# Performance work log

Hardware: AMD Instinct MI355X
Metric: run time of the kernel (lower is better)

The kernel has to match this reference:

```python
import jax, jax.numpy as jnp
import numpy as np

B, N, D, H_IMG, W_IMG = 1, 6, 128, 28, 60
HB, WB = 50, 50
HEADS, DH = 4, 32
INNER = HEADS * DH  # 128 == D
Q = HB * WB
NK = N * H_IMG * W_IMG


def _ln(x, w, b, eps=1e-5):
    m = jnp.mean(x, axis=-1, keepdims=True)
    v = jnp.var(x, axis=-1, keepdims=True)
    return (x - m) * jax.lax.rsqrt(v + eps) * w + b


def setup_inputs() -> dict:
    key = jax.random.key(0)
    ks = jax.random.split(key, 20)
    s = 0.02
    inp = {
        "q": jax.random.normal(ks[0], (B, D, HB, WB), jnp.float32),
        "k": jax.random.normal(ks[1], (B, N, D, H_IMG, W_IMG), jnp.float32),
        "v": jax.random.normal(ks[2], (B, N, D, H_IMG, W_IMG), jnp.float32),
        "W_logits": jax.random.uniform(ks[3], (B, Q, NK), jnp.float32),
        "vis_flat": jax.random.randint(ks[4], (B, Q, NK), 0, 2).astype(jnp.int32),
        "skip": jax.random.normal(ks[5], (B, D, HB, WB), jnp.float32),
        # LayerNorm params
        "qn_w": jnp.ones((D,), jnp.float32), "qn_b": jnp.zeros((D,), jnp.float32),
        "kn_w": jnp.ones((D,), jnp.float32), "kn_b": jnp.zeros((D,), jnp.float32),
        "vn_w": jnp.ones((D,), jnp.float32), "vn_b": jnp.zeros((D,), jnp.float32),
        "pre_w": jnp.ones((D,), jnp.float32), "pre_b": jnp.zeros((D,), jnp.float32),
        "post_w": jnp.ones((D,), jnp.float32), "post_b": jnp.zeros((D,), jnp.float32),
        # Linear params, stored [in, out]
        "wq": jax.random.normal(ks[6], (D, INNER), jnp.float32) * s,
        "bq": jnp.zeros((INNER,), jnp.float32),
        "wk": jax.random.normal(ks[7], (D, INNER), jnp.float32) * s,
        "bk": jnp.zeros((INNER,), jnp.float32),
        "wv": jax.random.normal(ks[8], (D, INNER), jnp.float32) * s,
        "bv": jnp.zeros((INNER,), jnp.float32),
        "wp": jax.random.normal(ks[9], (INNER, D), jnp.float32) * s,
        "bp": jnp.zeros((D,), jnp.float32),
        "w1": jax.random.normal(ks[10], (D, 2 * D), jnp.float32) * s,
        "b1": jnp.zeros((2 * D,), jnp.float32),
        "w2": jax.random.normal(ks[11], (2 * D, D), jnp.float32) * s,
        "b2": jnp.zeros((D,), jnp.float32),
    }
    return inp


def reference(q, k, v, W_logits, vis_flat, skip,
              qn_w, qn_b, kn_w, kn_b, vn_w, vn_b, pre_w, pre_b, post_w, post_b,
              wq, bq, wk, bk, wv, bv, wp, bp, w1, b1, w2, b2):
    b, d, Hb, Wb = q.shape
    _, n, _, hi, wi = k.shape
    Qn = Hb * Wb
    # b d H W -> b (H W) d ; b n d h w -> b (n h w) d
    qf = q.reshape(b, d, Qn).transpose(0, 2, 1)
    kf = k.transpose(0, 1, 3, 4, 2).reshape(b, n * hi * wi, d)
    vf = v.transpose(0, 1, 3, 4, 2).reshape(b, n * hi * wi, d)
    qf = _ln(qf, qn_w, qn_b)
    kf = _ln(kf, kn_w, kn_b)
    vf = _ln(vf, vn_w, vn_b)
    qh = (qf @ wq + bq).reshape(b, Qn, HEADS, DH).transpose(0, 2, 1, 3)
    kh = (kf @ wk + bk).reshape(b, -1, HEADS, DH).transpose(0, 2, 1, 3)
    vh = (vf @ wv + bv).reshape(b, -1, HEADS, DH).transpose(0, 2, 1, 3)
    scale = DH ** (-0.5)
    logits = jnp.einsum('bhqd,bhkd->bhqk', qh, kh) * scale  # [b,h,Q,NK]
    neg_inf = jnp.finfo(logits.dtype).min
    logits = jnp.where(vis_flat[:, None] == 0, neg_inf, logits)
    logits = logits * W_logits[:, None]  # multiplicative EAF weighting
    attn = jax.nn.softmax(logits, axis=-1)
    out = jnp.einsum('bhqk,bhkd->bhqd', attn, vh)
    out = out.transpose(0, 2, 1, 3).reshape(b, Qn, INNER)
    out = out @ wp + bp
    z = out + skip.reshape(b, d, Qn).transpose(0, 2, 1)
    z = _ln(z, pre_w, pre_b)
    z = z + (jax.nn.gelu(z @ w1 + b1, approximate=False) @ w2 + b2)
    z = _ln(z, post_w, post_b)
    return z.transpose(0, 2, 1).reshape(b, d, Hb, Wb)
```

## Files before the change

### kernel.cpp

```cpp
#include <hip/hip_runtime.h>
#include <hip/hip_bf16.h>
#include <math.h>

typedef short short8 __attribute__((ext_vector_type(8)));
typedef float floatx4 __attribute__((ext_vector_type(4)));
typedef int   intx4  __attribute__((ext_vector_type(4)));

#define D 128
#define Q 2500
#define QPAD 2560
#define NK 10080
#define NKPAD 10112
#define SPLITS 19
#define CPS 17
#define OPS 163904
#define LPS 10304
#define VBW 320
#define VROW 40
#define QSCALE 0.25501268426834347f
#define NEGBIG -3.0e38f

__device__ __forceinline__ unsigned short f2bf(float f) {
    unsigned u = __float_as_uint(f);
    unsigned r = (u + 0x7fffu + ((u >> 16) & 1u)) >> 16;
    return (unsigned short)r;
}
__device__ __forceinline__ unsigned pack2bf(float lo, float hi) {
    unsigned u0 = __float_as_uint(lo) + 0x8000u;
    unsigned u1 = __float_as_uint(hi) + 0x8000u;
    return (u0 >> 16) | (u1 & 0xffff0000u);
}
__device__ __forceinline__ float bflo(unsigned u) { return __uint_as_float(u << 16); }
__device__ __forceinline__ float bfhi(unsigned u) { return __uint_as_float(u & 0xffff0000u); }

__global__ __launch_bounds__(256) void prep_kernel(
    const float* __restrict__ qi, const float* __restrict__ ki, const float* __restrict__ vi,
    const float* __restrict__ qw, const float* __restrict__ qb_,
    const float* __restrict__ kw, const float* __restrict__ kb,
    const float* __restrict__ vw, const float* __restrict__ vb,
    unsigned short* __restrict__ xq, unsigned short* __restrict__ xk,
    unsigned short* __restrict__ xv,
    const float* __restrict__ wq, const float* __restrict__ wk,
    const float* __restrict__ wv, const float* __restrict__ wp,
    const float* __restrict__ w1, const float* __restrict__ w2,
    unsigned short* __restrict__ wqT, unsigned short* __restrict__ wkT,
    unsigned short* __restrict__ wvT, unsigned short* __restrict__ wpT,
    unsigned short* __restrict__ w1T, unsigned short* __restrict__ w2T,
    const int* __restrict__ vis, unsigned* __restrict__ vbits) {
    int bid = blockIdx.x, t = threadIdx.x;
    if (bid >= 1227) {
        int row = bid - 1227;
        const int* src = vis + (size_t)row * NK;
        #pragma unroll 2
        for (int w = t; w < 315; w += 256) {
            unsigned bits = 0;
            const intx4* p = (const intx4*)(src + w * 32);
            #pragma unroll
            for (int g = 0; g < 8; g++) {
                intx4 v = p[g];
                #pragma unroll
                for (int j = 0; j < 4; j++) bits |= (v[j] ? 1u : 0u) << (g * 4 + j);
            }
            vbits[(size_t)row * VBW + w] = bits;
        }
        return;
    }
    if (bid >= 715) {
        int idx = (bid - 715) * 256 + t;
        if (idx < 49152) {
            int m = idx >> 14;
            int local = idx & 16383;
            int n = local >> 7, kk = local & 127;
            const float* w = (m == 0) ? wq : ((m == 1) ? wk : wv);
            unsigned short* o = (m == 0) ? wqT : ((m == 1) ? wkT : wvT);
            o[local] = f2bf(w[kk * 128 + n]);
        } else if (idx < 65536) {
            int local = idx - 49152;
            int n = local >> 7, kk = local & 127;
            wpT[local] = f2bf(wp[kk * 128 + n]);
        } else if (idx < 98304) {
            int local = idx - 65536;
            int n = local >> 7, kk = local & 127;
            w1T[local] = f2bf(w1[kk * 256 + n]);
        } else {
            int local = idx - 98304;
            int n = local >> 8, kk = local & 255;
            w2T[local] = f2bf(w2[kk * 128 + n]);
        }
        return;
    }
    __shared__ float lds2[32 * 132];
    const float* src; unsigned short* dst; const float *g, *b;
    int S, valid;
    if (bid < 79) {
        int p0 = bid * 32;
        src = qi + p0; S = Q; dst = xq + p0 * D; g = qw; b = qb_;
        valid = Q - p0; if (valid > 32) valid = 32;
    } else if (bid < 397) {
        int tt = bid - 79;
        int n = tt / 53, tile = tt - n * 53, r = tile * 32;
        src = ki + (size_t)(n * 128) * 1680 + r; S = 1680;
        dst = xk + (n * 1680 + r) * D; g = kw; b = kb;
        valid = 1680 - r; if (valid > 32) valid = 32;
    } else {
        int tt = bid - 397;
        int n = tt / 53, tile = tt - n * 53, r = tile * 32;
        src = vi + (size_t)(n * 128) * 1680 + r; S = 1680;
        dst = xv + (n * 1680 + r) * D; g = vw; b = vb;
        valid = 1680 - r; if (valid > 32) valid = 32;
    }
    #pragma unroll
    for (int pass = 0; pass < 4; pass++) {
        int s = pass * 256 + t;
        int d = s >> 3, ps = s & 7;
        floatx4 val = {0.f, 0.f, 0.f, 0.f};
        if (ps * 4 < valid) val = *(const floatx4*)(src + (size_t)d * S + ps * 4);
        #pragma unroll
        for (int j = 0; j < 4; j++) lds2[(ps * 4 + j) * 132 + d] = val[j];
    }
    __syncthreads();
    int lane = t & 63, wvx = t >> 6;
    int pos = wvx * 8 + (lane >> 3), l7 = lane & 7;
    floatx4 x4[4];
    #pragma unroll
    for (int k = 0; k < 4; k++) x4[k] = *(const floatx4*)(&lds2[pos * 132 + l7 * 16 + k * 4]);
    float s = 0.f, ss = 0.f;
    #pragma unroll
    for (int k = 0; k < 4; k++)
        #pragma unroll
        for (int j = 0; j < 4; j++) { s += x4[k][j]; ss += x4[k][j] * x4[k][j]; }
    #pragma unroll
    for (int m = 1; m <= 4; m <<= 1) { s += __shfl_xor(s, m, 64); ss += __shfl_xor(ss, m, 64); }
    float mean = s * (1.0f / 128.0f);
    float var = ss * (1.0f / 128.0f) - mean * mean;
    float rstd = rsqrtf(var + 1e-5f);
    short8 o1, o2;
    #pragma unroll
    for (int k = 0; k < 4; k++) {
        floatx4 g4 = *(const floatx4*)(g + l7 * 16 + k * 4);
        floatx4 b4 = *(const floatx4*)(b + l7 * 16 + k * 4);
        #pragma unroll
        for (int j = 0; j < 4; j++) {
            float o = (x4[k][j] - mean) * rstd * g4[j] + b4[j];
            if (k < 2) o1[k * 4 + j] = (short)f2bf(o);
            else o2[(k - 2) * 4 + j] = (short)f2bf(o);
        }
    }
    if (pos < valid) {
        *(short8*)(dst + pos * D + l7 * 16) = o1;
        *(short8*)(dst + pos * D + l7 * 16 + 8) = o2;
    }
}

__global__ __launch_bounds__(256) void proj_kernel(
    const unsigned short* __restrict__ xq, const unsigned short* __restrict__ xk,
    const unsigned short* __restrict__ xv,
    const unsigned short* __restrict__ wqT, const unsigned short* __restrict__ wkT,
    const unsigned short* __restrict__ wvT,
    const float* __restrict__ bq, const float* __restrict__ bk, const float* __restrict__ bv,
    unsigned short* __restrict__ qh, unsigned short* __restrict__ kh,
    unsigned short* __restrict__ vhT) {
    __shared__ short vlds[128 * 72];
    int bid = blockIdx.x;
    const unsigned short *src, *wT; const float* bias; int mb, mode; float scale;
    if (bid < 40)       { mode = 0; src = xq; wT = wqT; bias = bq; mb = bid * 64; scale = QSCALE; }
    else if (bid < 198) { mode = 1; src = xk; wT = wkT; bias = bk; mb = (bid - 40) * 64; scale = 1.0f; }
    else                { mode = 2; src = xv; wT = wvT; bias = bv; mb = (bid - 198) * 64; scale = 1.0f; }
    int t = threadIdx.x, wave = t >> 6, lane = t & 63;
    int l15 = lane & 15, quad = lane >> 4;
    int m0 = mb + wave * 16;
    floatx4 acc[8];
    #pragma unroll
    for (int i = 0; i < 8; i++) acc[i] = (floatx4){0.f, 0.f, 0.f, 0.f};
    #pragma unroll
    for (int kf = 0; kf < 4; kf++) {
        short8 A = *(const short8*)(src + (m0 + l15) * D + kf * 32 + quad * 8);
        #pragma unroll
        for (int nt = 0; nt < 8; nt++) {
            short8 Bv = *(const short8*)(wT + (nt * 16 + l15) * D + kf * 32 + quad * 8);
            acc[nt] = __builtin_amdgcn_mfma_f32_16x16x32_bf16(A, Bv, acc[nt], 0, 0, 0);
        }
    }
    if (mode != 2) {
        unsigned short* dst = (mode == 0) ? qh : kh;
        #pragma unroll
        for (int nt = 0; nt < 8; nt++) {
            float bb = bias[nt * 16 + l15];
            #pragma unroll
            for (int r = 0; r < 4; r++)
                dst[(m0 + quad * 4 + r) * D + nt * 16 + l15] = f2bf((acc[nt][r] + bb) * scale);
        }
    } else {
        #pragma unroll
        for (int nt = 0; nt < 8; nt++) {
            float bb = bias[nt * 16 + l15];
            #pragma unroll
            for (int r = 0; r < 4; r++)
                vlds[(nt * 16 + l15) * 72 + (wave * 16 + quad * 4 + r)] =
                    (short)f2bf(acc[nt][r] + bb);
        }
        __syncthreads();
        int pr = t & 31, dd = t >> 5;
        int sub = pr >> 4, i = pr & 15;
        #pragma unroll
        for (int pass = 0; pass < 16; pass++) {
            int d = pass * 8 + dd;
            unsigned lo = (unsigned short)vlds[d * 72 + sub * 32 + i];
            unsigned hi = (unsigned short)vlds[d * 72 + sub * 32 + 16 + i];
            *(unsigned*)(vhT + (size_t)d * NKPAD + mb + sub * 32 + 2 * i) = lo | (hi << 16);
        }
    }
}

template<int USEBITS>
__global__ __launch_bounds__(256, 3) void attn_kernel_t(
    const unsigned short* __restrict__ qh, const unsigned short* __restrict__ kh,
    const unsigned short* __restrict__ vhT,
    const float* __restrict__ Wl, const int* __restrict__ vis,
    const unsigned* __restrict__ vbits,
    unsigned* __restrict__ OpartU, float* __restrict__ lpart) {
    __shared__ short Kl[2][32 * 136];
    __shared__ short Vl[2][128 * VROW];
    __shared__ unsigned Pl[4][16 * 18];
    int bid = blockIdx.x;
    int split = bid % SPLITS, qt = bid / SPLITS;
    int t = threadIdx.x, wave = t >> 6, lane = t & 63;
    int l15 = lane & 15, quad = lane >> 4;
    int qb = qt * 64 + wave * 16;
    int k00 = split * (CPS * 32);
    int cmax = (NK - k00) >> 5; if (cmax > CPS) cmax = CPS;

    short8 qB[4];
    #pragma unroll
    for (int h = 0; h < 4; h++)
        qB[h] = *(const short8*)(qh + (size_t)(qb + l15) * D + h * 32 + quad * 8);

    int kr = t >> 3, ks = (t & 7) * 2;
    int vd = t >> 1, vs = (t & 1) * 2;
    const uint4* ksrc = (const uint4*)(kh + (size_t)(k00 + kr) * D + ks * 8);
    const uint4* vsrc = (const uint4*)(vhT + (size_t)vd * NKPAD + k00 + vs * 8);
    short* kdst = &Kl[0][kr * 136 + ks * 8];
    short* vdst = &Vl[0][vd * VROW + vs * 8];

    int wrow = qb + l15; if (wrow >= Q) wrow = Q - 1;
    const float* wp = Wl + (size_t)wrow * NK + k00 + quad * 4;
    const int*   vp = vis + (size_t)wrow * NK + k00 + quad * 4;
    const unsigned* vbp = vbits + (size_t)wrow * VBW + split * CPS;

    const floatx4 zf = {0.f, 0.f, 0.f, 0.f};
    floatx4 O[4][2];
    float lacc[4];
    #pragma unroll
    for (int h = 0; h < 4; h++) { O[h][0] = zf; O[h][1] = zf; lacc[h] = 0.f; }

    uint4 ka = ksrc[0], kb2 = ksrc[1];
    uint4 va = vsrc[0], vb2 = vsrc[1];
    floatx4 wc0 = *(const floatx4*)wp;
    floatx4 wc1 = *(const floatx4*)(wp + 16);
    intx4 vc0, vc1;
    unsigned vbc = 0;
    if constexpr (USEBITS) {
        vbc = vbp[0];
    } else {
        vc0 = *(const intx4*)vp;
        vc1 = *(const intx4*)(vp + 16);
    }
    *(uint4*)kdst = ka;       *(uint4*)(kdst + 8) = kb2;
    *(uint4*)vdst = va;       *(uint4*)(vdst + 8) = vb2;

    unsigned* pw = Pl[wave];
    #pragma unroll 1
    for (int c = 0; c < cmax; c++) {
        __syncthreads();
        int buf = c & 1;
        uint4 nka, nkb, nva, nvb;
        floatx4 wn0, wn1; intx4 vn0, vn1;
        unsigned vbn = 0;
        if (c + 1 < cmax) {
            const uint4* ks2 = ksrc + (size_t)(c + 1) * 512;
            const uint4* vs2 = vsrc + (size_t)(c + 1) * 4;
            nka = ks2[0]; nkb = ks2[1];
            nva = vs2[0]; nvb = vs2[1];
            wn0 = *(const floatx4*)(wp + (c + 1) * 32);
            wn1 = *(const floatx4*)(wp + (c + 1) * 32 + 16);
            if constexpr (USEBITS) {
                vbn = vbp[c + 1];
            } else {
                vn0 = *(const intx4*)(vp + (c + 1) * 32);
                vn1 = *(const intx4*)(vp + (c + 1) * 32 + 16);
            }
        }
        float a2[8], b2[8];
        if constexpr (USEBITS) {
            unsigned bq = vbc >> (quad * 4);
            #pragma unroll
            for (int r = 0; r < 4; r++) {
                bool m0 = (bq >> r) & 1u;
                bool m1 = (bq >> (16 + r)) & 1u;
                a2[r]     = m0 ? wc0[r] : 0.f;
                b2[r]     = m0 ? 0.f : wc0[r] * NEGBIG;
                a2[4 + r] = m1 ? wc1[r] : 0.f;
                b2[4 + r] = m1 ? 0.f : wc1[r] * NEGBIG;
            }
        } else {
            #pragma unroll
            for (int r = 0; r < 4; r++) {
                a2[r]     = vc0[r] ? wc0[r] : 0.f;
                b2[r]     = vc0[r] ? 0.f : wc0[r] * NEGBIG;
                a2[4 + r] = vc1[r] ? wc1[r] : 0.f;
                b2[4 + r] = vc1[r] ? 0.f : wc1[r] * NEGBIG;
            }
        }
        const short* Kb = Kl[buf];
        const short* Vb = Vl[buf];
        #pragma unroll
        for (int h = 0; h < 4; h++) {
            short8 kA0 = *(const short8*)(Kb + l15 * 136 + h * 32 + quad * 8);
            short8 kA1 = *(const short8*)(Kb + (16 + l15) * 136 + h * 32 + quad * 8);
            floatx4 S0 = __builtin_amdgcn_mfma_f32_16x16x32_bf16(kA0, qB[h], zf, 0, 0, 0);
            floatx4 S1 = __builtin_amdgcn_mfma_f32_16x16x32_bf16(kA1, qB[h], zf, 0, 0, 0);
            float p0[4], p1[4];
            #pragma unroll
            for (int r = 0; r < 4; r++) {
                p0[r] = exp2f(S0[r] * a2[r] + b2[r]);
                p1[r] = exp2f(S1[r] * a2[4 + r] + b2[4 + r]);
                lacc[h] += p0[r] + p1[r];
            }
            pw[(quad * 2) * 18 + l15]     = pack2bf(p0[0], p0[1]);
            pw[(quad * 2 + 1) * 18 + l15] = pack2bf(p0[2], p0[3]);
            pw[(8 + quad * 2) * 18 + l15]     = pack2bf(p1[0], p1[1]);
            pw[(8 + quad * 2 + 1) * 18 + l15] = pack2bf(p1[2], p1[3]);
            union { unsigned u[4]; short8 s8; } pb;
            #pragma unroll
            for (int jj = 0; jj < 4; jj++)
                pb.u[jj] = pw[(quad * 4 + jj) * 18 + l15];
            short8 vA0 = *(const short8*)(Vb + (h * 32 + l15) * VROW + quad * 8);
            short8 vA1 = *(const short8*)(Vb + (h * 32 + 16 + l15) * VROW + quad * 8);
            O[h][0] = __builtin_amdgcn_mfma_f32_16x16x32_bf16(vA0, pb.s8, O[h][0], 0, 0, 0);
            O[h][1] = __builtin_amdgcn_mfma_f32_16x16x32_bf16(vA1, pb.s8, O[h][1], 0, 0, 0);
        }
        if (c + 1 < cmax) {
            short* kd = buf ? kdst : (kdst + 32 * 136);
            short* vd2 = buf ? vdst : (vdst + 128 * VROW);
            *(uint4*)kd = nka;       *(uint4*)(kd + 8) = nkb;
            *(uint4*)vd2 = nva;      *(uint4*)(vd2 + 8) = nvb;
            wc0 = wn0; wc1 = wn1;
            if constexpr (USEBITS) { vbc = vbn; }
            else { vc0 = vn0; vc1 = vn1; }
        }
    }

    int row = qb + l15;
    #pragma unroll
    for (int h = 0; h < 4; h++) {
        float lv = lacc[h];
        lv += __shfl_xor(lv, 16, 64);
        lv += __shfl_xor(lv, 32, 64);
        if (quad == 0) lpart[(size_t)split * LPS + row * 4 + h] = lv;
        #pragma unroll
        for (int tl = 0; tl < 2; tl++) {
            uint2 o2;
            o2.x = pack2bf(O[h][tl][0], O[h][tl][1]);
            o2.y = pack2bf(O[h][tl][2], O[h][tl][3]);
            *(uint2*)(OpartU + (size_t)split * OPS + ((size_t)row * 4 + h) * 16 + tl * 8 + quad * 2) = o2;
        }
    }
}

__global__ __launch_bounds__(128) void combine_kernel(
    const unsigned* __restrict__ Opart, const float* __restrict__ lpart,
    unsigned* __restrict__ A1u) {
    int tid = blockIdx.x * 128 + threadIdx.x;
    int sl = tid & 3, he = (tid >> 2) & 3, grow = tid >> 4;
    float lsum = 0.f;
    #pragma unroll 5
    for (int sp = 0; sp < SPLITS; sp++) lsum += lpart[(size_t)sp * LPS + grow * 4 + he];
    float inv = 1.0f / fmaxf(lsum, 1e-30f);
    size_t base = ((size_t)grow * 4 + he) * 16 + sl * 4;
    float a0 = 0.f, a1 = 0.f, a2 = 0.f, a3 = 0.f, a4 = 0.f, a5 = 0.f, a6 = 0.f, a7 = 0.f;
    #pragma unroll 5
    for (int sp = 0; sp < SPLITS; sp++) {
        uint4 u = *(const uint4*)(Opart + (size_t)sp * OPS + base);
        a0 += bflo(u.x); a1 += bfhi(u.x);
        a2 += bflo(u.y); a3 += bfhi(u.y);
        a4 += bflo(u.z); a5 += bfhi(u.z);
        a6 += bflo(u.w); a7 += bfhi(u.w);
    }
    uint4 o;
    o.x = pack2bf(a0 * inv, a1 * inv);
    o.y = pack2bf(a2 * inv, a3 * inv);
    o.z = pack2bf(a4 * inv, a5 * inv);
    o.w = pack2bf(a6 * inv, a7 * inv);
    *(uint4*)(A1u + (size_t)grow * 64 + he * 16 + sl * 4) = o;
}

__global__ __launch_bounds__(256) void mlp_kernel(
    const unsigned short* __restrict__ A1,
    const unsigned short* __restrict__ wpT,
    const float* __restrict__ bp, const float* __restrict__ skip,
    const float* __restrict__ pre_w, const float* __restrict__ pre_b,
    const unsigned short* __restrict__ w1T, const float* __restrict__ b1,
    const unsigned short* __restrict__ w2T, const float* __restrict__ b2,
    const float* __restrict__ post_w, const float* __restrict__ post_b,
    float* __restrict__ out) {
    __shared__ __align__(16) char smem[51200];
    short* Z1 = (short*)smem;
    short* H1 = (short*)(smem + 17408);
    float* Zout = (float*)smem;

    int qb = blockIdx.x * 64;
    int t = threadIdx.x, wave = t >> 6, lane = t & 63;
    int l15 = lane & 15, quad = lane >> 4;
    int m0 = wave * 16;

    floatx4 z[8];
    #pragma unroll
    for (int i = 0; i < 8; i++) z[i] = (floatx4){0.f, 0.f, 0.f, 0.f};
    #pragma unroll
    for (int kf = 0; kf < 4; kf++) {
        short8 A = *(const short8*)(A1 + (size_t)(qb + m0 + l15) * 128 + kf * 32 + quad * 8);
        #pragma unroll
        for (int nt = 0; nt < 8; nt++) {
            short8 Bv = *(const short8*)(wpT + (nt * 16 + l15) * D + kf * 32 + quad * 8);
            z[nt] = __builtin_amdgcn_mfma_f32_16x16x32_bf16(A, Bv, z[nt], 0, 0, 0);
        }
    }
    float Zv[8][4];
    #pragma unroll
    for (int nt = 0; nt < 8; nt++) {
        int n = nt * 16 + l15;
        float bb = bp[n];
        #pragma unroll
        for (int r = 0; r < 4; r++) {
            int q = qb + m0 + quad * 4 + r;
            int qc = q < Q ? q : (Q - 1);
            Zv[nt][r] = z[nt][r] + bb + skip[n * Q + qc];
        }
    }
    float Zn[8][4];
    {
        #pragma unroll
        for (int r = 0; r < 4; r++) {
            float s1 = 0.f, s2 = 0.f;
            #pragma unroll
            for (int nt = 0; nt < 8; nt++) { s1 += Zv[nt][r]; s2 += Zv[nt][r] * Zv[nt][r]; }
            #pragma unroll
            for (int m = 1; m <= 8; m <<= 1) { s1 += __shfl_xor(s1, m, 64); s2 += __shfl_xor(s2, m, 64); }
            float mean = s1 * (1.0f / 128.0f);
            float var = s2 * (1.0f / 128.0f) - mean * mean;
            float rstd = rsqrtf(var + 1e-5f);
            #pragma unroll
            for (int nt = 0; nt < 8; nt++) Zn[nt][r] = (Zv[nt][r] - mean) * rstd;
        }
        #pragma unroll
        for (int nt = 0; nt < 8; nt++) {
            int n = nt * 16 + l15;
            float g = pre_w[n], be = pre_b[n];
            #pragma unroll
            for (int r = 0; r < 4; r++) {
                Zn[nt][r] = Zn[nt][r] * g + be;
                Z1[(m0 + quad * 4 + r) * 136 + n] = (short)f2bf(Zn[nt][r]);
            }
        }
    }
    {
        floatx4 h2[16];
        #pragma unroll
        for (int i = 0; i < 16; i++) h2[i] = (floatx4){0.f, 0.f, 0.f, 0.f};
        #pragma unroll
        for (int kf = 0; kf < 4; kf++) {
            short8 A = *(const short8*)(Z1 + (m0 + l15) * 136 + kf * 32 + quad * 8);
            #pragma unroll
            for (int nt = 0; nt < 16; nt++) {
                short8 Bv = *(const short8*)(w1T + (nt * 16 + l15) * D + kf * 32 + quad * 8);
                h2[nt] = __builtin_amdgcn_mfma_f32_16x16x32_bf16(A, Bv, h2[nt], 0, 0, 0);
            }
        }
        #pragma unroll
        for (int nt = 0; nt < 16; nt++) {
            int n = nt * 16 + l15;
            float bb = b1[n];
            #pragma unroll
            for (int r = 0; r < 4; r++) {
                float x = h2[nt][r] + bb;
                float gl = 0.5f * x * (1.0f + erff(x * 0.70710678118654752f));
                H1[(m0 + quad * 4 + r) * 264 + n] = (short)f2bf(gl);
            }
        }
    }
    floatx4 o3[8];
    #pragma unroll
    for (int i = 0; i < 8; i++) o3[i] = (floatx4){0.f, 0.f, 0.f, 0.f};
    #pragma unroll
    for (int kf = 0; kf < 8; kf++) {
        short8 A = *(const short8*)(H1 + (m0 + l15) * 264 + kf * 32 + quad * 8);
        #pragma unroll
        for (int nt = 0; nt < 8; nt++) {
            short8 Bv = *(const short8*)(w2T + (nt * 16 + l15) * 256 + kf * 32 + quad * 8);
            o3[nt] = __builtin_amdgcn_mfma_f32_16x16x32_bf16(A, Bv, o3[nt], 0, 0, 0);
        }
    }
    float Z2[8][4];
    #pragma unroll
    for (int nt = 0; nt < 8; nt++) {
        int n = nt * 16 + l15;
        float bb = b2[n];
        #pragma unroll
        for (int r = 0; r < 4; r++) Z2[nt][r] = Zn[nt][r] + o3[nt][r] + bb;
    }
    float Zo[8][4];
    {
        #pragma unroll
        for (int r = 0; r < 4; r++) {
            float s1 = 0.f, s2 = 0.f;
            #pragma unroll
            for (int nt = 0; nt < 8; nt++) { s1 += Z2[nt][r]; s2 += Z2[nt][r] * Z2[nt][r]; }
            #pragma unroll
            for (int m = 1; m <= 8; m <<= 1) { s1 += __shfl_xor(s1, m, 64); s2 += __shfl_xor(s2, m, 64); }
            float mean = s1 * (1.0f / 128.0f);
            float var = s2 * (1.0f / 128.0f) - mean * mean;
            float rstd = rsqrtf(var + 1e-5f);
            #pragma unroll
            for (int nt = 0; nt < 8; nt++) Zo[nt][r] = (Z2[nt][r] - mean) * rstd;
        }
        #pragma unroll
        for (int nt = 0; nt < 8; nt++) {
            int n = nt * 16 + l15;
            float g = post_w[n], be = post_b[n];
            #pragma unroll
            for (int r = 0; r < 4; r++) Zo[nt][r] = Zo[nt][r] * g + be;
        }
    }
    __syncthreads();
    #pragma unroll
    for (int nt = 0; nt < 8; nt++)
        #pragma unroll
        for (int r = 0; r < 4; r++)
            Zout[(nt * 16 + l15) * 65 + m0 + quad * 4 + r] = Zo[nt][r];
    __syncthreads();
    {
        int pl = t & 63;
        int q = qb + pl;
        if (q < Q) {
            #pragma unroll
            for (int it = 0; it < 32; it++) {
                int n = it * 4 + (t >> 6);
                out[n * Q + q] = Zout[n * 65 + pl];
            }
        }
    }
}

extern "C" void kernel_launch(void* const* d_in, const int* in_sizes, int n_in,
                              void* d_out, int out_size, void* d_ws, size_t ws_size,
                              hipStream_t stream) {
    (void)in_sizes; (void)n_in; (void)out_size;
    const float* q      = (const float*)d_in[0];
    const float* k      = (const float*)d_in[1];
    const float* v      = (const float*)d_in[2];
    const float* Wl     = (const float*)d_in[3];
    const int*   vis    = (const int*)  d_in[4];
    const float* skip   = (const float*)d_in[5];
    const float* qn_w   = (const float*)d_in[6];
    const float* qn_b   = (const float*)d_in[7];
    const float* kn_w   = (const float*)d_in[8];
    const float* kn_b   = (const float*)d_in[9];
    const float* vn_w   = (const float*)d_in[10];
    const float* vn_b   = (const float*)d_in[11];
    const float* pre_w  = (const float*)d_in[12];
    const float* pre_b  = (const float*)d_in[13];
    const float* post_w = (const float*)d_in[14];
    const float* post_b = (const float*)d_in[15];
    const float* wq     = (const float*)d_in[16];
    const float* bq     = (const float*)d_in[17];
    const float* wk     = (const float*)d_in[18];
    const float* bk     = (const float*)d_in[19];
    const float* wv     = (const float*)d_in[20];
    const float* bv     = (const float*)d_in[21];
    const float* wp     = (const float*)d_in[22];
    const float* bp     = (const float*)d_in[23];
    const float* w1     = (const float*)d_in[24];
    const float* b1     = (const float*)d_in[25];
    const float* w2     = (const float*)d_in[26];
    const float* b2     = (const float*)d_in[27];
    float* out = (float*)d_out;

    char* ws = (char*)d_ws;
    unsigned short* xq  = (unsigned short*)(ws + 0);
    unsigned short* xk  = (unsigned short*)(ws + 655360);
    unsigned short* xv  = (unsigned short*)(ws + 3244032);
    unsigned short* qh  = (unsigned short*)(ws + 5832704);
    unsigned short* kh  = (unsigned short*)(ws + 6488064);
    unsigned short* vhT = (unsigned short*)(ws + 9076736);
    unsigned short* wqT = (unsigned short*)(ws + 11665408);
    unsigned short* wkT = (unsigned short*)(ws + 11698176);
    unsigned short* wvT = (unsigned short*)(ws + 11730944);
    unsigned short* wpT = (unsigned short*)(ws + 11763712);
    unsigned short* w1T = (unsigned short*)(ws + 11796480);
    unsigned short* w2T = (unsigned short*)(ws + 11862016);
    unsigned* OpartU    = (unsigned*)(ws + 11927552);
    float* lpart        = (float*)(ws + 34874112);
    unsigned* vbits     = (unsigned*)(ws + 36316672);
    unsigned* A1u       = (unsigned*)(ws + 0);

    const bool usebits = (ws_size == 0) || (ws_size >= 39520000ull);

    prep_kernel<<<dim3(usebits ? 3727 : 1227), dim3(256), 0, stream>>>(
        q, k, v, qn_w, qn_b, kn_w, kn_b, vn_w, vn_b, xq, xk, xv,
        wq, wk, wv, wp, w1, w2, wqT, wkT, wvT, wpT, w1T, w2T, vis, vbits);
    proj_kernel<<<dim3(356), dim3(256), 0, stream>>>(xq, xk, xv, wqT, wkT, wvT, bq, bk, bv,
                                                     qh, kh, vhT);
    if (usebits)
        attn_kernel_t<1><<<dim3(40 * SPLITS), dim3(256), 0, stream>>>(
            qh, kh, vhT, Wl, vis, vbits, OpartU, lpart);
    else
        attn_kernel_t<0><<<dim3(40 * SPLITS), dim3(256), 0, stream>>>(
            qh, kh, vhT, Wl, vis, vbits, OpartU, lpart);
    combine_kernel<<<dim3(320), dim3(128), 0, stream>>>(OpartU, lpart, A1u);
    mlp_kernel<<<dim3(40), dim3(256), 0, stream>>>((const unsigned short*)A1u, wpT, bp, skip,
                                                   pre_w, pre_b, w1T, b1, w2T, b2,
                                                   post_w, post_b, out);
}
```

Baseline: 364.5 us.

## Shuffle P tile in registers and fuse split-combine into MLP kernel

In the attention loop, the per-wave LDS round trip that turned the P tile into an MFMA operand is replaced by hardware bf16 pack instructions and cross-lane shuffles. The separate combine kernel that reduces split partials is folded into the MLP kernel, which reduces into LDS before the projection GEMM. This drops one kernel launch and a global round trip for A1. The trade-off is that the combine now runs on only 40 blocks, which lowers parallelism for that reduction, and the MLP kernel needs more LDS.

```diff
diff --git a/kernel.cpp b/kernel.cpp
--- a/kernel.cpp
+++ b/kernel.cpp
@@ -29,6 +29,11 @@
     unsigned u0 = __float_as_uint(lo) + 0x8000u;
     unsigned u1 = __float_as_uint(hi) + 0x8000u;
     return (u0 >> 16) | (u1 & 0xffff0000u);
+}
+__device__ __forceinline__ unsigned cvtpk(float lo, float hi) {
+    unsigned r;
+    asm("v_cvt_pk_bf16_f32 %0, %1, %2" : "=v"(r) : "v"(lo), "v"(hi));
+    return r;
 }
 __device__ __forceinline__ float bflo(unsigned u) { return __uint_as_float(u << 16); }
 __device__ __forceinline__ float bfhi(unsigned u) { return __uint_as_float(u & 0xffff0000u); }
@@ -221,7 +226,6 @@
     unsigned* __restrict__ OpartU, float* __restrict__ lpart) {
     __shared__ short Kl[2][32 * 136];
     __shared__ short Vl[2][128 * VROW];
-    __shared__ unsigned Pl[4][16 * 18];
     int bid = blockIdx.x;
     int split = bid % SPLITS, qt = bid / SPLITS;
     int t = threadIdx.x, wave = t >> 6, lane = t & 63;
@@ -246,6 +250,10 @@
     const float* wp = Wl + (size_t)wrow * NK + k00 + quad * 4;
     const int*   vp = vis + (size_t)wrow * NK + k00 + quad * 4;
     const unsigned* vbp = vbits + (size_t)wrow * VBW + split * CPS;
+
+    int idxA = l15 + ((quad & 1) << 5);
+    int idxB = idxA + 16;
+    bool hiK = (quad >= 2);
 
     const floatx4 zf = {0.f, 0.f, 0.f, 0.f};
     floatx4 O[4][2];
@@ -268,7 +276,6 @@
     *(uint4*)kdst = ka;       *(uint4*)(kdst + 8) = kb2;
     *(uint4*)vdst = va;       *(uint4*)(vdst + 8) = vb2;
 
-    unsigned* pw = Pl[wave];
     #pragma unroll 1
     for (int c = 0; c < cmax; c++) {
         __syncthreads();
@@ -326,14 +333,19 @@
                 p1[r] = exp2f(S1[r] * a2[4 + r] + b2[4 + r]);
                 lacc[h] += p0[r] + p1[r];
             }
-            pw[(quad * 2) * 18 + l15]     = pack2bf(p0[0], p0[1]);
-            pw[(quad * 2 + 1) * 18 + l15] = pack2bf(p0[2], p0[3]);
-            pw[(8 + quad * 2) * 18 + l15]     = pack2bf(p1[0], p1[1]);
-            pw[(8 + quad * 2 + 1) * 18 + l15] = pack2bf(p1[2], p1[3]);
+            unsigned u0 = cvtpk(p0[0], p0[1]);
+            unsigned u1 = cvtpk(p0[2], p0[3]);
+            unsigned u2 = cvtpk(p1[0], p1[1]);
+            unsigned u3 = cvtpk(p1[2], p1[3]);
+            unsigned s0A = __shfl(u0, idxA, 64), s2A = __shfl(u2, idxA, 64);
+            unsigned s1A = __shfl(u1, idxA, 64), s3A = __shfl(u3, idxA, 64);
+            unsigned s0B = __shfl(u0, idxB, 64), s2B = __shfl(u2, idxB, 64);
+            unsigned s1B = __shfl(u1, idxB, 64), s3B = __shfl(u3, idxB, 64);
             union { unsigned u[4]; short8 s8; } pb;
-            #pragma unroll
-            for (int jj = 0; jj < 4; jj++)
-                pb.u[jj] = pw[(quad * 4 + jj) * 18 + l15];
+            pb.u[0] = hiK ? s2A : s0A;
+            pb.u[1] = hiK ? s3A : s1A;
+            pb.u[2] = hiK ? s2B : s0B;
+            pb.u[3] = hiK ? s3B : s1B;
             short8 vA0 = *(const short8*)(Vb + (h * 32 + l15) * VROW + quad * 8);
             short8 vA1 = *(const short8*)(Vb + (h * 32 + 16 + l15) * VROW + quad * 8);
             O[h][0] = __builtin_amdgcn_mfma_f32_16x16x32_bf16(vA0, pb.s8, O[h][0], 0, 0, 0);
@@ -360,42 +372,15 @@
         #pragma unroll
         for (int tl = 0; tl < 2; tl++) {
             uint2 o2;
-            o2.x = pack2bf(O[h][tl][0], O[h][tl][1]);
-            o2.y = pack2bf(O[h][tl][2], O[h][tl][3]);
+            o2.x = cvtpk(O[h][tl][0], O[h][tl][1]);
+            o2.y = cvtpk(O[h][tl][2], O[h][tl][3]);
             *(uint2*)(OpartU + (size_t)split * OPS + ((size_t)row * 4 + h) * 16 + tl * 8 + quad * 2) = o2;
         }
     }
 }
 
-__global__ __launch_bounds__(128) void combine_kernel(
+__global__ __launch_bounds__(256) void mlp_kernel(
     const unsigned* __restrict__ Opart, const float* __restrict__ lpart,
-    unsigned* __restrict__ A1u) {
-    int tid = blockIdx.x * 128 + threadIdx.x;
-    int sl = tid & 3, he = (tid >> 2) & 3, grow = tid >> 4;
-    float lsum = 0.f;
-    #pragma unroll 5
-    for (int sp = 0; sp < SPLITS; sp++) lsum += lpart[(size_t)sp * LPS + grow * 4 + he];
-    float inv = 1.0f / fmaxf(lsum, 1e-30f);
-    size_t base = ((size_t)grow * 4 + he) * 16 + sl * 4;
-    float a0 = 0.f, a1 = 0.f, a2 = 0.f, a3 = 0.f, a4 = 0.f, a5 = 0.f, a6 = 0.f, a7 = 0.f;
-    #pragma unroll 5
-    for (int sp = 0; sp < SPLITS; sp++) {
-        uint4 u = *(const uint4*)(Opart + (size_t)sp * OPS + base);
-        a0 += bflo(u.x); a1 += bfhi(u.x);
-        a2 += bflo(u.y); a3 += bfhi(u.y);
-        a4 += bflo(u.z); a5 += bfhi(u.z);
-        a6 += bflo(u.w); a7 += bfhi(u.w);
-    }
-    uint4 o;
-    o.x = pack2bf(a0 * inv, a1 * inv);
-    o.y = pack2bf(a2 * inv, a3 * inv);
-    o.z = pack2bf(a4 * inv, a5 * inv);
-    o.w = pack2bf(a6 * inv, a7 * inv);
-    *(uint4*)(A1u + (size_t)grow * 64 + he * 16 + sl * 4) = o;
-}
-
-__global__ __launch_bounds__(256) void mlp_kernel(
-    const unsigned short* __restrict__ A1,
     const unsigned short* __restrict__ wpT,
     const float* __restrict__ bp, const float* __restrict__ skip,
     const float* __restrict__ pre_w, const float* __restrict__ pre_b,
@@ -403,22 +388,52 @@
     const unsigned short* __restrict__ w2T, const float* __restrict__ b2,
     const float* __restrict__ post_w, const float* __restrict__ post_b,
     float* __restrict__ out) {
-    __shared__ __align__(16) char smem[51200];
-    short* Z1 = (short*)smem;
-    short* H1 = (short*)(smem + 17408);
-    float* Zout = (float*)smem;
+    __shared__ __align__(16) char smem[68608];
+    short* A1l = (short*)smem;
+    short* Z1 = (short*)(smem + 17408);
+    short* H1 = (short*)(smem + 34816);
+    float* Zout = (float*)(smem + 17408);
+    unsigned* A1u = (unsigned*)smem;
 
     int qb = blockIdx.x * 64;
     int t = threadIdx.x, wave = t >> 6, lane = t & 63;
     int l15 = lane & 15, quad = lane >> 4;
     int m0 = wave * 16;
 
+    {
+        int row = t >> 2, he = t & 3;
+        int grow = qb + row;
+        float lsum = 0.f;
+        #pragma unroll 5
+        for (int sp = 0; sp < SPLITS; sp++) lsum += lpart[(size_t)sp * LPS + grow * 4 + he];
+        float inv = 1.0f / fmaxf(lsum, 1e-30f);
+        size_t base = ((size_t)grow * 4 + he) * 16;
+        #pragma unroll
+        for (int sl = 0; sl < 4; sl++) {
+            float a0 = 0.f, a1 = 0.f, a2 = 0.f, a3 = 0.f, a4 = 0.f, a5 = 0.f, a6 = 0.f, a7 = 0.f;
+            #pragma unroll 5
+            for (int sp = 0; sp < SPLITS; sp++) {
+                uint4 u = *(const uint4*)(Opart + (size_t)sp * OPS + base + sl * 4);
+                a0 += bflo(u.x); a1 += bfhi(u.x);
+                a2 += bflo(u.y); a3 += bfhi(u.y);
+                a4 += bflo(u.z); a5 += bfhi(u.z);
+                a6 += bflo(u.w); a7 += bfhi(u.w);
+            }
+            int o = row * 68 + he * 16 + sl * 4;
+            A1u[o + 0] = pack2bf(a0 * inv, a1 * inv);
+            A1u[o + 1] = pack2bf(a2 * inv, a3 * inv);
+            A1u[o + 2] = pack2bf(a4 * inv, a5 * inv);
+            A1u[o + 3] = pack2bf(a6 * inv, a7 * inv);
+        }
+    }
+    __syncthreads();
+
     floatx4 z[8];
     #pragma unroll
     for (int i = 0; i < 8; i++) z[i] = (floatx4){0.f, 0.f, 0.f, 0.f};
     #pragma unroll
     for (int kf = 0; kf < 4; kf++) {
-        short8 A = *(const short8*)(A1 + (size_t)(qb + m0 + l15) * 128 + kf * 32 + quad * 8);
+        short8 A = *(const short8*)(A1l + (m0 + l15) * 136 + kf * 32 + quad * 8);
         #pragma unroll
         for (int nt = 0; nt < 8; nt++) {
             short8 Bv = *(const short8*)(wpT + (nt * 16 + l15) * D + kf * 32 + quad * 8);
@@ -601,7 +616,6 @@
     unsigned* OpartU    = (unsigned*)(ws + 11927552);
     float* lpart        = (float*)(ws + 34874112);
     unsigned* vbits     = (unsigned*)(ws + 36316672);
-    unsigned* A1u       = (unsigned*)(ws + 0);
 
     const bool usebits = (ws_size == 0) || (ws_size >= 39520000ull);
 
@@ -616,8 +630,7 @@
     else
         attn_kernel_t<0><<<dim3(40 * SPLITS), dim3(256), 0, stream>>>(
             qh, kh, vhT, Wl, vis, vbits, OpartU, lpart);
-    combine_kernel<<<dim3(320), dim3(128), 0, stream>>>(OpartU, lpart, A1u);
-    mlp_kernel<<<dim3(40), dim3(256), 0, stream>>>((const unsigned short*)A1u, wpT, bp, skip,
+    mlp_kernel<<<dim3(40), dim3(256), 0, stream>>>(OpartU, lpart, wpT, bp, skip,
                                                    pre_w, pre_b, w1T, b1, w2T, b2,
                                                    post_w, post_b, out);
 }
```

New measurement: 368.2 us. About the same (+1.0%).

## Replace LDS P transpose with lane shuffles, prefetch weights two chunks ahead

Applied to the files above, without the earlier changes.

The attention kernel now redistributes the probability tile into the MFMA B-operand layout with cross-lane shuffles (ds_bpermute) instead of writing to and reading back from a per-wave LDS buffer. The shared P buffer is gone. Packing to bf16 now uses the hardware v_cvt_pk_bf16_f32 instruction. In the bitmask path, the W_logits and visibility-bit loads are prefetched two chunks ahead to hide global latency. The MFMA/exp section is wrapped in s_setprio. These changes trade LDS traffic and a dependency for extra shuffles, more live registers, and possible occupancy pressure.

```diff
diff --git a/kernel.cpp b/kernel.cpp
--- a/kernel.cpp
+++ b/kernel.cpp
@@ -29,6 +29,11 @@
     unsigned u0 = __float_as_uint(lo) + 0x8000u;
     unsigned u1 = __float_as_uint(hi) + 0x8000u;
     return (u0 >> 16) | (u1 & 0xffff0000u);
+}
+__device__ __forceinline__ unsigned cvtpk(float lo, float hi) {
+    unsigned r;
+    asm("v_cvt_pk_bf16_f32 %0, %1, %2" : "=v"(r) : "v"(lo), "v"(hi));
+    return r;
 }
 __device__ __forceinline__ float bflo(unsigned u) { return __uint_as_float(u << 16); }
 __device__ __forceinline__ float bfhi(unsigned u) { return __uint_as_float(u & 0xffff0000u); }
@@ -221,7 +226,6 @@
     unsigned* __restrict__ OpartU, float* __restrict__ lpart) {
     __shared__ short Kl[2][32 * 136];
     __shared__ short Vl[2][128 * VROW];
-    __shared__ unsigned Pl[4][16 * 18];
     int bid = blockIdx.x;
     int split = bid % SPLITS, qt = bid / SPLITS;
     int t = threadIdx.x, wave = t >> 6, lane = t & 63;
@@ -247,6 +251,10 @@
     const int*   vp = vis + (size_t)wrow * NK + k00 + quad * 4;
     const unsigned* vbp = vbits + (size_t)wrow * VBW + split * CPS;
 
+    int idxA = l15 + ((quad & 1) << 5);
+    int idxB = idxA + 16;
+    bool hiK = (quad >= 2);
+
     const floatx4 zf = {0.f, 0.f, 0.f, 0.f};
     floatx4 O[4][2];
     float lacc[4];
@@ -257,10 +265,14 @@
     uint4 va = vsrc[0], vb2 = vsrc[1];
     floatx4 wc0 = *(const floatx4*)wp;
     floatx4 wc1 = *(const floatx4*)(wp + 16);
+    floatx4 wn0, wn1;
     intx4 vc0, vc1;
-    unsigned vbc = 0;
+    unsigned vbc = 0, vbn = 0;
     if constexpr (USEBITS) {
         vbc = vbp[0];
+        wn0 = *(const floatx4*)(wp + 32);
+        wn1 = *(const floatx4*)(wp + 48);
+        vbn = vbp[1];
     } else {
         vc0 = *(const intx4*)vp;
         vc1 = *(const intx4*)(vp + 16);
@@ -268,24 +280,29 @@
     *(uint4*)kdst = ka;       *(uint4*)(kdst + 8) = kb2;
     *(uint4*)vdst = va;       *(uint4*)(vdst + 8) = vb2;
 
-    unsigned* pw = Pl[wave];
     #pragma unroll 1
     for (int c = 0; c < cmax; c++) {
         __syncthreads();
         int buf = c & 1;
         uint4 nka, nkb, nva, nvb;
-        floatx4 wn0, wn1; intx4 vn0, vn1;
-        unsigned vbn = 0;
+        floatx4 w20, w21; intx4 vn0, vn1;
+        unsigned vb2n = 0;
         if (c + 1 < cmax) {
             const uint4* ks2 = ksrc + (size_t)(c + 1) * 512;
             const uint4* vs2 = vsrc + (size_t)(c + 1) * 4;
             nka = ks2[0]; nkb = ks2[1];
             nva = vs2[0]; nvb = vs2[1];
-            wn0 = *(const floatx4*)(wp + (c + 1) * 32);
-            wn1 = *(const floatx4*)(wp + (c + 1) * 32 + 16);
-            if constexpr (USEBITS) {
-                vbn = vbp[c + 1];
-            } else {
+        }
+        if constexpr (USEBITS) {
+            if (c + 2 < cmax) {
+                w20 = *(const floatx4*)(wp + (c + 2) * 32);
+                w21 = *(const floatx4*)(wp + (c + 2) * 32 + 16);
+                vb2n = vbp[c + 2];
+            }
+        } else {
+            if (c + 1 < cmax) {
+                wn0 = *(const floatx4*)(wp + (c + 1) * 32);
+                wn1 = *(const floatx4*)(wp + (c + 1) * 32 + 16);
                 vn0 = *(const intx4*)(vp + (c + 1) * 32);
                 vn1 = *(const intx4*)(vp + (c + 1) * 32 + 16);
             }
@@ -313,6 +330,7 @@
         }
         const short* Kb = Kl[buf];
         const short* Vb = Vl[buf];
+        __builtin_amdgcn_s_setprio(1);
         #pragma unroll
         for (int h = 0; h < 4; h++) {
             short8 kA0 = *(const short8*)(Kb + l15 * 136 + h * 32 + quad * 8);
@@ -326,27 +344,36 @@
                 p1[r] = exp2f(S1[r] * a2[4 + r] + b2[4 + r]);
                 lacc[h] += p0[r] + p1[r];
             }
-            pw[(quad * 2) * 18 + l15]     = pack2bf(p0[0], p0[1]);
-            pw[(quad * 2 + 1) * 18 + l15] = pack2bf(p0[2], p0[3]);
-            pw[(8 + quad * 2) * 18 + l15]     = pack2bf(p1[0], p1[1]);
-            pw[(8 + quad * 2 + 1) * 18 + l15] = pack2bf(p1[2], p1[3]);
+            unsigned u0 = cvtpk(p0[0], p0[1]);
+            unsigned u1 = cvtpk(p0[2], p0[3]);
+            unsigned u2 = cvtpk(p1[0], p1[1]);
+            unsigned u3 = cvtpk(p1[2], p1[3]);
+            unsigned s0A = __shfl(u0, idxA, 64), s2A = __shfl(u2, idxA, 64);
+            unsigned s1A = __shfl(u1, idxA, 64), s3A = __shfl(u3, idxA, 64);
+            unsigned s0B = __shfl(u0, idxB, 64), s2B = __shfl(u2, idxB, 64);
+            unsigned s1B = __shfl(u1, idxB, 64), s3B = __shfl(u3, idxB, 64);
             union { unsigned u[4]; short8 s8; } pb;
-            #pragma unroll
-            for (int jj = 0; jj < 4; jj++)
-                pb.u[jj] = pw[(quad * 4 + jj) * 18 + l15];
+            pb.u[0] = hiK ? s2A : s0A;
+            pb.u[1] = hiK ? s3A : s1A;
+            pb.u[2] = hiK ? s2B : s0B;
+            pb.u[3] = hiK ? s3B : s1B;
             short8 vA0 = *(const short8*)(Vb + (h * 32 + l15) * VROW + quad * 8);
             short8 vA1 = *(const short8*)(Vb + (h * 32 + 16 + l15) * VROW + quad * 8);
             O[h][0] = __builtin_amdgcn_mfma_f32_16x16x32_bf16(vA0, pb.s8, O[h][0], 0, 0, 0);
             O[h][1] = __builtin_amdgcn_mfma_f32_16x16x32_bf16(vA1, pb.s8, O[h][1], 0, 0, 0);
         }
+        __builtin_amdgcn_s_setprio(0);
         if (c + 1 < cmax) {
             short* kd = buf ? kdst : (kdst + 32 * 136);
             short* vd2 = buf ? vdst : (vdst + 128 * VROW);
             *(uint4*)kd = nka;       *(uint4*)(kd + 8) = nkb;
             *(uint4*)vd2 = nva;      *(uint4*)(vd2 + 8) = nvb;
-            wc0 = wn0; wc1 = wn1;
-            if constexpr (USEBITS) { vbc = vbn; }
-            else { vc0 = vn0; vc1 = vn1; }
+        }
+        if constexpr (USEBITS) {
+            wc0 = wn0; wc1 = wn1; vbc = vbn;
+            if (c + 2 < cmax) { wn0 = w20; wn1 = w21; vbn = vb2n; }
+        } else {
+            if (c + 1 < cmax) { wc0 = wn0; wc1 = wn1; vc0 = vn0; vc1 = vn1; }
         }
     }
 
@@ -360,8 +387,8 @@
         #pragma unroll
         for (int tl = 0; tl < 2; tl++) {
             uint2 o2;
-            o2.x = pack2bf(O[h][tl][0], O[h][tl][1]);
-            o2.y = pack2bf(O[h][tl][2], O[h][tl][3]);
+            o2.x = cvtpk(O[h][tl][0], O[h][tl][1]);
+            o2.y = cvtpk(O[h][tl][2], O[h][tl][3]);
             *(uint2*)(OpartU + (size_t)split * OPS + ((size_t)row * 4 + h) * 16 + tl * 8 + quad * 2) = o2;
         }
     }
```

Measured after the change: 360.2 us. Within noise of the previous version (-1.2%).
